# Kernel optimization log

Hardware: AMD Instinct MI355X
Metric: run time of the kernel (lower is better)

## Reference

```python
import jax, jax.numpy as jnp
import numpy as np

B, C, H, W = 32, 256, 32, 32


def setup_inputs() -> dict:
    key = jax.random.key(0)
    k1, k2, k3 = jax.random.split(key, 3)
    h = jax.random.normal(k1, (B, C, H, W), dtype=jnp.float32)
    w1_w = jax.random.normal(k2, (1, C), dtype=jnp.float32) * (1.0 / np.sqrt(C))
    w1_b = jnp.zeros((1,), dtype=jnp.float32)
    w2_w = jax.random.normal(k3, (1, C), dtype=jnp.float32) * (1.0 / np.sqrt(C))
    w2_b = jnp.zeros((1,), dtype=jnp.float32)
    return {"h": h, "w1_w": w1_w, "w1_b": w1_b, "w2_w": w2_w, "w2_b": w2_b}


def reference(h, w1_w, w1_b, w2_w, w2_b):
    b, c, hh, ww = h.shape
    x = jnp.transpose(h, (0, 2, 3, 1))            # [B,H,W,C]
    # scalar projections of every spatial token
    a = jnp.einsum('bhwc,c->bhw', x, w1_w[0]) + w1_b[0]   # query-side scalar [B,H,W]
    k = jnp.einsum('bhwc,c->bhw', x, w2_w[0]) + w2_b[0]   # key-side scalar   [B,H,W]
    n = hh * ww
    # additive attention scores over all spatial pairs: [B,H,W,HW]
    scores = jnp.tanh(a[:, :, :, None] + k.reshape(b, 1, 1, n))
    attn = jax.nn.softmax(scores, axis=-1)                 # exp(tanh)/sum == softmax(tanh)
    ctx = jnp.einsum('bijn,bnc->bijc', attn, x.reshape(b, n, c))  # [B,H,W,C]
    out = jnp.where(ctx >= 0, ctx, 0.2 * ctx)              # LeakyReLU(0.2)
    return jnp.transpose(out, (0, 3, 1, 2))                # [B,C,H,W]
```

## Files before the change

kernel.cpp:

```cpp
#include <hip/hip_runtime.h>

constexpr int Bn = 32;
constexpr int Cn = 256;
constexpr int Nn = 1024;

constexpr float C2 = 2.8853900817779268f;
constexpr float K1 = 1.4426950408889634f;

typedef __bf16 v8bf  __attribute__((ext_vector_type(8)));
typedef float  v16f  __attribute__((ext_vector_type(16)));


__global__ __launch_bounds__(256) void prep_kernel(
    const float* __restrict__ h,
    const float* __restrict__ w1, const float* __restrict__ w1b,
    const float* __restrict__ w2, const float* __restrict__ w2b,
    float* __restrict__ pa_g, float* __restrict__ q_g,
    unsigned char* __restrict__ hbf)
{
    int blk = blockIdx.x;
    int xcd = blk & 7, idx = blk >> 3;
    int b   = xcd * 4 + (idx >> 4);
    int n0  = (idx & 15) * 64;
    int t = threadIdx.x, w = t >> 6, l = t & 63;

    __shared__ float lds_t[64][68];
    __shared__ float p1[4][64], p2[4][64];

    const float* hb = h + (size_t)b * Cn * Nn + n0;
    float s1 = 0.f, s2 = 0.f;

    int nt32  = (n0 >> 5) + (w >> 1);
    int gbase = (w & 1) * 2;
    unsigned char* nt_base = hbf + (size_t)(b * 32 + nt32) * 16384;

    for (int chunk = 0; chunk < 4; ++chunk) {
        if (chunk) __syncthreads();
#pragma unroll 4
        for (int ci = 0; ci < 16; ++ci) {
            int c = chunk * 64 + w * 16 + ci;
            float v = hb[(size_t)c * Nn + l];
            s1 = fmaf(v, w1[c], s1);
            s2 = fmaf(v, w2[c], s2);
            lds_t[w * 16 + ci][l] = v;
        }
        __syncthreads();
        int c = chunk * 64 + l;
        unsigned char* crow = nt_base + c * 64;
#pragma unroll
        for (int g2 = 0; g2 < 2; ++g2) {
            int g = gbase + g2;
            int col = (w >> 1) * 32 + g * 8;
            float4 va = *(const float4*)&lds_t[l][col];
            float4 vb = *(const float4*)&lds_t[l][col + 4];
            union { __bf16 bx[8]; uint4 u4; } pk;
            pk.bx[0] = (__bf16)va.x; pk.bx[1] = (__bf16)va.y;
            pk.bx[2] = (__bf16)va.z; pk.bx[3] = (__bf16)va.w;
            pk.bx[4] = (__bf16)vb.x; pk.bx[5] = (__bf16)vb.y;
            pk.bx[6] = (__bf16)vb.z; pk.bx[7] = (__bf16)vb.w;
            *(uint4*)(crow + ((g ^ (c & 3)) << 4)) = pk.u4;
        }
    }

    p1[w][l] = s1;
    p2[w][l] = s2;
    __syncthreads();
    if (t < 64) {
        float a = p1[0][t] + p1[1][t] + p1[2][t] + p1[3][t] + w1b[0];
        float k = p2[0][t] + p2[1][t] + p2[2][t] + p2[3][t] + w2b[0];
        pa_g[b * Nn + n0 + t] = exp2f(C2 * a);
        q_g [b * Nn + n0 + t] = exp2f(C2 * k);
    }
}

constexpr int EST_OFF  = 0;
constexpr int QS_OFF   = 8192;
constexpr int SP_OFF   = 65792;
constexpr int SINV_OFF = 67840;
constexpr int CTX_SMEM = 68096;

__global__ __launch_bounds__(512, 4) void ctx_kernel(
    const unsigned char* __restrict__ hbf,
    const float* __restrict__ pa_g, const float* __restrict__ q_g,
    float* __restrict__ out)
{
    __shared__ alignas(16) unsigned char smem[CTX_SMEM];
    float* qs           = (float*)(smem + QS_OFF);
    float (*Sp)[64]     = (float(*)[64])(smem + SP_OFF);
    float* Sinv         = (float*)(smem + SINV_OFF);
    float (*comb)[257]  = (float(*)[257])smem;

    int blk = blockIdx.x;
    int xcd = blk & 7, slot = blk >> 3;
    int b   = xcd * 4 + (slot >> 4);
    int i0  = (slot & 15) * 64;

    int t = threadIdx.x, w = t >> 6, l = t & 63;
    int lm = l & 31, lh = l >> 5;
    int cq = w & 3, wq = w >> 2;

    const unsigned char* hbf_b = hbf + (size_t)b * 524288;

    for (int i = t; i < Nn; i += 512) qs[i] = q_g[b * Nn + i];
    float pav = pa_g[b * Nn + i0 + l];

    v16f acc[2][2];
#pragma unroll
    for (int x = 0; x < 2; ++x)
#pragma unroll
        for (int y = 0; y < 2; ++y)
#pragma unroll
            for (int r = 0; r < 16; ++r) acc[x][y][r] = 0.f;
    float Spart = 0.f;

    unsigned char* estw = smem + EST_OFF + l * 128 + ((w ^ (l & 7)) << 4);

    int cB   = cq * 64 + lm;
    int m4   = cB & 3;
    int off0 = cB * 64 + ((lh ^ m4) << 4);
    int off1 = cB * 64 + (((2 + lh) ^ m4) << 4);

    for (int tt = 0; tt < 16; ++tt) {
        __syncthreads();
        const unsigned char* pt = hbf_b + (size_t)((wq << 4) + tt) * 16384;
        v8bf b00 = *(const v8bf*)(pt + off0);
        v8bf b01 = *(const v8bf*)(pt + off0 + 2048);
        v8bf b10 = *(const v8bf*)(pt + off1);
        v8bf b11 = *(const v8bf*)(pt + off1 + 2048);
        {
            int qb = wq * 512 + tt * 32 + cq * 8;
            float4 q0 = *(const float4*)&qs[qb];
            float4 q1 = *(const float4*)&qs[qb + 4];
            float qv[8] = {q0.x, q0.y, q0.z, q0.w, q1.x, q1.y, q1.z, q1.w};
            v8bf ev;
#pragma unroll
            for (int j = 0; j < 8; ++j) {
                float z = pav * qv[j];
                float r = __builtin_amdgcn_rcpf(1.f + z);
                float e = exp2f(fmaf(r, -2.f * K1, K1));
                __bf16 eb = (__bf16)e;
                ev[j] = eb;
                Spart += (float)eb;
            }
            *(v8bf*)estw = ev;
        }
        __syncthreads();
#pragma unroll
        for (int ks = 0; ks < 2; ++ks) {
            int gA = ((wq << 2) + (ks << 1) + lh) ^ (lm & 7);
            v8bf a0 = *(const v8bf*)(smem + EST_OFF + lm * 128        + (gA << 4));
            v8bf a1 = *(const v8bf*)(smem + EST_OFF + (32 + lm) * 128 + (gA << 4));
            v8bf b0 = ks ? b10 : b00;
            v8bf b1 = ks ? b11 : b01;
            acc[0][0] = __builtin_amdgcn_mfma_f32_32x32x16_bf16(a0, b0, acc[0][0], 0, 0, 0);
            acc[0][1] = __builtin_amdgcn_mfma_f32_32x32x16_bf16(a0, b1, acc[0][1], 0, 0, 0);
            acc[1][0] = __builtin_amdgcn_mfma_f32_32x32x16_bf16(a1, b0, acc[1][0], 0, 0, 0);
            acc[1][1] = __builtin_amdgcn_mfma_f32_32x32x16_bf16(a1, b1, acc[1][1], 0, 0, 0);
        }
    }

    Sp[w][l] = Spart;
    __syncthreads();
    if (t < 64) {
        float S = 0.f;
#pragma unroll
        for (int ww = 0; ww < 8; ++ww) S += Sp[ww][t];
        Sinv[t] = 1.f / S;
    }
    if (wq == 1) {
#pragma unroll
        for (int x = 0; x < 2; ++x)
#pragma unroll
            for (int y = 0; y < 2; ++y)
#pragma unroll
                for (int r = 0; r < 16; ++r) {
                    int rl = (r & 3) + 8 * (r >> 2) + 4 * lh;
                    comb[x * 32 + rl][cq * 64 + y * 32 + lm] = acc[x][y][r];
                }
    }
    __syncthreads();
    if (wq == 0) {
#pragma unroll
        for (int x = 0; x < 2; ++x)
#pragma unroll
            for (int y = 0; y < 2; ++y)
#pragma unroll
                for (int r = 0; r < 16; ++r) {
                    int rl  = (r & 3) + 8 * (r >> 2) + 4 * lh;
                    int row = x * 32 + rl;
                    int col = cq * 64 + y * 32 + lm;
                    float v = (acc[x][y][r] + comb[row][col]) * Sinv[row];
                    v = (v >= 0.f) ? v : 0.2f * v;
                    comb[row][col] = v;
                }
    }
    __syncthreads();
    float* ob = out + (size_t)b * Cn * Nn + i0;
#pragma unroll
    for (int p = 0; p < 8; ++p) {
        int slot = t + (p << 9);
        int c    = slot >> 4;
        int i4   = (slot & 15) << 2;
        float4 o;
        o.x = comb[i4 + 0][c];
        o.y = comb[i4 + 1][c];
        o.z = comb[i4 + 2][c];
        o.w = comb[i4 + 3][c];
        *(float4*)(ob + (size_t)c * Nn + i4) = o;
    }
}

extern "C" void kernel_launch(void* const* d_in, const int* in_sizes, int n_in,
                              void* d_out, int out_size, void* d_ws, size_t ws_size,
                              hipStream_t stream) {
    const float* h   = (const float*)d_in[0];
    const float* w1w = (const float*)d_in[1];
    const float* w1b = (const float*)d_in[2];
    const float* w2w = (const float*)d_in[3];
    const float* w2b = (const float*)d_in[4];
    float* out = (float*)d_out;

    float* pa_ws = (float*)d_ws;
    float* q_ws  = pa_ws + Bn * Nn;
    unsigned char* hbf = (unsigned char*)d_ws + 262144;

    prep_kernel<<<512, 256, 0, stream>>>(h, w1w, w1b, w2w, w2b, pa_ws, q_ws, hbf);
    ctx_kernel <<<512, 512, 0, stream>>>(hbf, pa_ws, q_ws, out);
}
```

Measured before the change: 119.9 us.

## Double-buffer score tile in ctx kernel and widen prep kernel to 512 threads

The ctx kernel now alternates between two LDS buffers for the exp-score tile, which removes one of the two barriers per iteration. The qs region is moved up to make room for the second buffer. The prep kernel doubles its block size to 512 threads and handles 128 channels per chunk in two chunks instead of four, giving more memory-level parallelism and fewer barriers. The cost is more LDS per block in both kernels, plus some risk of a race if the write into the buffer a lagging wave is still reading is not properly ordered.

```diff
diff --git a/kernel.cpp b/kernel.cpp
--- a/kernel.cpp
+++ b/kernel.cpp
@@ -11,7 +11,7 @@
 typedef float  v16f  __attribute__((ext_vector_type(16)));
 
 
-__global__ __launch_bounds__(256) void prep_kernel(
+__global__ __launch_bounds__(512) void prep_kernel(
     const float* __restrict__ h,
     const float* __restrict__ w1, const float* __restrict__ w1b,
     const float* __restrict__ w2, const float* __restrict__ w2b,
@@ -24,35 +24,38 @@
     int n0  = (idx & 15) * 64;
     int t = threadIdx.x, w = t >> 6, l = t & 63;
 
-    __shared__ float lds_t[64][68];
-    __shared__ float p1[4][64], p2[4][64];
+    __shared__ float lds_t[128][68];
+    __shared__ float p1[8][64], p2[8][64];
 
     const float* hb = h + (size_t)b * Cn * Nn + n0;
     float s1 = 0.f, s2 = 0.f;
 
-    int nt32  = (n0 >> 5) + (w >> 1);
+    int ccP   = (w >> 2) * 64 + l;
+    int ntl   = (w >> 1) & 1;
     int gbase = (w & 1) * 2;
+    int nt32  = (n0 >> 5) + ntl;
     unsigned char* nt_base = hbf + (size_t)(b * 32 + nt32) * 16384;
 
-    for (int chunk = 0; chunk < 4; ++chunk) {
+    for (int chunk = 0; chunk < 2; ++chunk) {
         if (chunk) __syncthreads();
-#pragma unroll 4
+#pragma unroll 8
         for (int ci = 0; ci < 16; ++ci) {
-            int c = chunk * 64 + w * 16 + ci;
+            int cc = w * 16 + ci;
+            int c  = chunk * 128 + cc;
             float v = hb[(size_t)c * Nn + l];
             s1 = fmaf(v, w1[c], s1);
             s2 = fmaf(v, w2[c], s2);
-            lds_t[w * 16 + ci][l] = v;
+            lds_t[cc][l] = v;
         }
         __syncthreads();
-        int c = chunk * 64 + l;
+        int c = chunk * 128 + ccP;
         unsigned char* crow = nt_base + c * 64;
 #pragma unroll
         for (int g2 = 0; g2 < 2; ++g2) {
-            int g = gbase + g2;
-            int col = (w >> 1) * 32 + g * 8;
-            float4 va = *(const float4*)&lds_t[l][col];
-            float4 vb = *(const float4*)&lds_t[l][col + 4];
+            int g   = gbase + g2;
+            int col = ntl * 32 + g * 8;
+            float4 va = *(const float4*)&lds_t[ccP][col];
+            float4 vb = *(const float4*)&lds_t[ccP][col + 4];
             union { __bf16 bx[8]; uint4 u4; } pk;
             pk.bx[0] = (__bf16)va.x; pk.bx[1] = (__bf16)va.y;
             pk.bx[2] = (__bf16)va.z; pk.bx[3] = (__bf16)va.w;
@@ -66,15 +69,16 @@
     p2[w][l] = s2;
     __syncthreads();
     if (t < 64) {
-        float a = p1[0][t] + p1[1][t] + p1[2][t] + p1[3][t] + w1b[0];
-        float k = p2[0][t] + p2[1][t] + p2[2][t] + p2[3][t] + w2b[0];
+        float a = w1b[0], k = w2b[0];
+#pragma unroll
+        for (int ww = 0; ww < 8; ++ww) { a += p1[ww][t]; k += p2[ww][t]; }
         pa_g[b * Nn + n0 + t] = exp2f(C2 * a);
         q_g [b * Nn + n0 + t] = exp2f(C2 * k);
     }
 }
 
 constexpr int EST_OFF  = 0;
-constexpr int QS_OFF   = 8192;
+constexpr int QS_OFF   = 16384;
 constexpr int SP_OFF   = 65792;
 constexpr int SINV_OFF = 67840;
 constexpr int CTX_SMEM = 68096;
@@ -113,15 +117,16 @@
             for (int r = 0; r < 16; ++r) acc[x][y][r] = 0.f;
     float Spart = 0.f;
 
-    unsigned char* estw = smem + EST_OFF + l * 128 + ((w ^ (l & 7)) << 4);
+    int est_sw = l * 128 + ((w ^ (l & 7)) << 4);
 
     int cB   = cq * 64 + lm;
     int m4   = cB & 3;
     int off0 = cB * 64 + ((lh ^ m4) << 4);
     int off1 = cB * 64 + (((2 + lh) ^ m4) << 4);
 
+    __syncthreads();
     for (int tt = 0; tt < 16; ++tt) {
-        __syncthreads();
+        unsigned char* est_base = smem + EST_OFF + ((tt & 1) << 13);
         const unsigned char* pt = hbf_b + (size_t)((wq << 4) + tt) * 16384;
         v8bf b00 = *(const v8bf*)(pt + off0);
         v8bf b01 = *(const v8bf*)(pt + off0 + 2048);
@@ -142,14 +147,14 @@
                 ev[j] = eb;
                 Spart += (float)eb;
             }
-            *(v8bf*)estw = ev;
+            *(v8bf*)(est_base + est_sw) = ev;
         }
         __syncthreads();
 #pragma unroll
         for (int ks = 0; ks < 2; ++ks) {
             int gA = ((wq << 2) + (ks << 1) + lh) ^ (lm & 7);
-            v8bf a0 = *(const v8bf*)(smem + EST_OFF + lm * 128        + (gA << 4));
-            v8bf a1 = *(const v8bf*)(smem + EST_OFF + (32 + lm) * 128 + (gA << 4));
+            v8bf a0 = *(const v8bf*)(est_base + lm * 128        + (gA << 4));
+            v8bf a1 = *(const v8bf*)(est_base + (32 + lm) * 128 + (gA << 4));
             v8bf b0 = ks ? b10 : b00;
             v8bf b1 = ks ? b11 : b01;
             acc[0][0] = __builtin_amdgcn_mfma_f32_32x32x16_bf16(a0, b0, acc[0][0], 0, 0, 0);
@@ -224,6 +229,6 @@
     float* q_ws  = pa_ws + Bn * Nn;
     unsigned char* hbf = (unsigned char*)d_ws + 262144;
 
-    prep_kernel<<<512, 256, 0, stream>>>(h, w1w, w1b, w2w, w2b, pa_ws, q_ws, hbf);
+    prep_kernel<<<512, 512, 0, stream>>>(h, w1w, w1b, w2w, w2b, pa_ws, q_ws, hbf);
     ctx_kernel <<<512, 512, 0, stream>>>(hbf, pa_ws, q_ws, out);
 }
```

Result: no change. 119.3 us (-0.5%).
